# Performance work log

Hardware: AMD Instinct MI355X
Metric: run time of the kernel (lower is better)

The kernel has to match this reference:

```python
import jax, jax.numpy as jnp
import numpy as np

D_MODEL = 1024
NUM_HEADS = 16
HEAD_DIM = D_MODEL // NUM_HEADS
THETA = 10000.0
B, S = 2, 2048


def _apply_rope(t, cos, sin):
    # t: [B, H, S, hd]; cos/sin: [S, hd//2]
    te = t[..., 0::2]
    to = t[..., 1::2]
    re = te * cos - to * sin
    ro = te * sin + to * cos
    out = jnp.stack([re, ro], axis=-1)  # [B,H,S,hd//2,2]
    return out.reshape(t.shape)


def setup_inputs() -> dict:
    key = jax.random.key(0)
    kx, kq, kk, kv, ko = jax.random.split(key, 5)
    std = 2.0 / (2 * D_MODEL) ** 0.5
    def w(k):
        return jnp.clip(std * jax.random.normal(k, (D_MODEL, D_MODEL), jnp.float32), -3.0 * std, 3.0 * std)
    return {
        "x": jax.random.normal(kx, (B, S, D_MODEL), jnp.float32),
        "Wq": w(kq),
        "Wk": w(kk),
        "Wv": w(kv),
        "Wo": w(ko),
    }


def reference(x, Wq, Wk, Wv, Wo):
    Bv, Sv, _ = x.shape
    def proj(W):
        return jnp.einsum('bsd,ed->bse', x, W).reshape(Bv, Sv, NUM_HEADS, HEAD_DIM).transpose(0, 2, 1, 3)
    q, k, v = proj(Wq), proj(Wk), proj(Wv)

    pos = jnp.arange(Sv, dtype=jnp.float32)
    inv_freq = THETA ** (-jnp.arange(0, HEAD_DIM, 2, dtype=jnp.float32) / HEAD_DIM)
    ang = pos[:, None] * inv_freq[None, :]  # [S, hd//2]
    cos, sin = jnp.cos(ang), jnp.sin(ang)
    q = _apply_rope(q, cos, sin)
    k = _apply_rope(k, cos, sin)

    scale = 1.0 / jnp.sqrt(jnp.float32(HEAD_DIM))
    scores = jnp.einsum('bhqd,bhkd->bhqk', q.astype(jnp.float32), k.astype(jnp.float32)) * scale
    causal = jnp.tril(jnp.ones((Sv, Sv), dtype=bool))
    scores = jnp.where(causal[None, None], scores, -jnp.inf)
    attn = jax.nn.softmax(scores, axis=-1)
    out = jnp.einsum('bhqk,bhkd->bhqd', attn, v.astype(jnp.float32))
    out = out.transpose(0, 2, 1, 3).reshape(Bv, Sv, D_MODEL)
    return jnp.einsum('bsd,ed->bse', out, Wo)
```

## Files before the change

### kernel.cpp

```cpp
#include <hip/hip_runtime.h>
#include <hip/hip_bf16.h>
#include <stdint.h>

typedef __bf16 bf16x8 __attribute__((ext_vector_type(8)));
typedef float  f32x4  __attribute__((ext_vector_type(4)));

__device__ __forceinline__ float bf2f(unsigned short u) {
    union { float f; uint32_t i; } v; v.i = ((uint32_t)u) << 16; return v.f;
}
__device__ __forceinline__ unsigned short f2bf(float f) {
    union { float f; uint32_t i; } v; v.f = f;
    uint32_t r = v.i + 0x7FFF + ((v.i >> 16) & 1);
    return (unsigned short)(r >> 16);
}
__device__ __forceinline__ unsigned short f2bf_rz(float f) {
    union { float f; uint32_t i; } v; v.f = f;
    return (unsigned short)(v.i >> 16);
}
__device__ __forceinline__ float exp2_raw(float x) {
    float r;
    asm("v_exp_f32 %0, %1" : "=v"(r) : "v"(x));
    return r;
}

#define GLD_LDS(gptr, lptr) \
    __builtin_amdgcn_global_load_lds( \
        (const __attribute__((address_space(1))) void*)(gptr), \
        (__attribute__((address_space(3))) void*)(lptr), 16, 0, 0)

__global__ __launch_bounds__(256) void convert_inputs(
    const void* __restrict__ x,  const void* __restrict__ wq,
    const void* __restrict__ wk, const void* __restrict__ wv,
    const void* __restrict__ wo, unsigned short* __restrict__ dst,
    unsigned short* __restrict__ wob_dst, int* __restrict__ flag)
{
    __shared__ int cnt[256];
    const int tid = threadIdx.x;
    uint32_t u = ((const uint32_t*)x)[tid];
    int e = (u >> 7) & 0xFF;
    cnt[tid] = (e >= 100 && e <= 140) ? 1 : 0;
    __syncthreads();
    for (int s = 128; s > 0; s >>= 1) {
        if (tid < s) cnt[tid] += cnt[tid + s];
        __syncthreads();
    }
    const int isf32 = (cnt[0] >= 128) ? 0 : 1;
    if (blockIdx.x == 0 && tid == 0) flag[0] = isf32 ? 0 : 1;

    int c = blockIdx.x * 256 + tid;
    const void* src; size_t off; unsigned short* out;
    if (c < 524288)      { src = x;  off = (size_t)c * 8;            out = dst + (size_t)c * 8; }
    else if (c < 655360) { src = wq; off = (size_t)(c - 524288) * 8; out = dst + (size_t)c * 8; }
    else if (c < 786432) { src = wk; off = (size_t)(c - 655360) * 8; out = dst + (size_t)c * 8; }
    else if (c < 917504) { src = wv; off = (size_t)(c - 786432) * 8; out = dst + (size_t)c * 8; }
    else                 { src = wo; off = (size_t)(c - 917504) * 8; out = wob_dst + off; }
    unsigned short t[8];
    if (isf32) {
        const float* s = (const float*)src + off;
        float4 f0 = *(const float4*)s;
        float4 f1 = *(const float4*)(s + 4);
        t[0] = f2bf(f0.x); t[1] = f2bf(f0.y); t[2] = f2bf(f0.z); t[3] = f2bf(f0.w);
        t[4] = f2bf(f1.x); t[5] = f2bf(f1.y); t[6] = f2bf(f1.z); t[7] = f2bf(f1.w);
    } else {
        *(uint4*)t = *(const uint4*)((const unsigned short*)src + off);
    }
    *(uint4*)out = *(const uint4*)t;
}

__global__ __launch_bounds__(512, 2) void gemm_qkv_8ph(
    const unsigned short* __restrict__ A,
    const unsigned short* __restrict__ B0,
    const unsigned short* __restrict__ B1,
    const unsigned short* __restrict__ B2,
    unsigned short* __restrict__ O0,
    unsigned short* __restrict__ O1,
    unsigned short* __restrict__ O2)
{
    __shared__ __align__(16) unsigned short Asl[2][16384];
    __shared__ __align__(16) unsigned short Bsl[2][16384];

    const int tid  = threadIdx.x;
    const int lane = tid & 63;
    const int wid  = tid >> 6;
    const int wm   = wid >> 2;
    const int wn   = wid & 3;
    const int lr   = lane & 15;
    const int quad = lane >> 4;

    const int bid   = blockIdx.x;
    const int xcd   = bid & 7;
    const int s_    = bid >> 3;
    const int m_idx = xcd + 8 * (s_ / 12);
    const int n_idx = s_ % 12;

    const int m0  = m_idx * 256;
    const int n0g = n_idx * 256;
    const int sel = n0g >> 10;
    const unsigned short* Bp = (sel == 0) ? B0 : ((sel == 1) ? B1 : B2);
    unsigned short* Optr     = (sel == 0) ? O0 : ((sel == 1) ? O1 : O2);
    const int n0  = n0g & 1023;

    const int sw0 = ((0 + quad) ^ (lr & 7)) * 8;
    const int sw1 = ((4 + quad) ^ (lr & 7)) * 8;

    f32x4 acc[2][4][2][2] = {};
    bf16x8 aF[4][2];
    bf16x8 bF[2][2];

#define STAGEA(T, H) do { \
    const int tA_ = (T); \
    _Pragma("unroll") \
    for (int p_ = 0; p_ < 2; ++p_) { \
        int c_   = p_ * 512 + tid; \
        int row_ = c_ >> 3; \
        int sc_  = ((c_ & 7) ^ (row_ & 7)) * 8; \
        GLD_LDS(&A[(size_t)(m0 + (H) * 128 + row_) * 1024 + tA_ * 64 + sc_], \
                &Asl[tA_ & 1][(H) * 8192 + c_ * 8]); \
    } } while (0)

#define STAGEB(T, H) do { \
    const int tB_ = (T); \
    _Pragma("unroll") \
    for (int p_ = 0; p_ < 2; ++p_) { \
        int c_   = p_ * 512 + tid; \
        int row_ = c_ >> 3; \
        int sc_  = ((c_ & 7) ^ (row_ & 7)) * 8; \
        GLD_LDS(&Bp[(size_t)(n0 + (H) * 128 + row_) * 1024 + tB_ * 64 + sc_], \
                &Bsl[tB_ & 1][(H) * 8192 + c_ * 8]); \
    } } while (0)

#define LOADA(BUF, QM) do { \
    _Pragma("unroll") \
    for (int fm_ = 0; fm_ < 4; ++fm_) { \
        const int row_ = (QM) * 128 + wm * 64 + fm_ * 16 + lr; \
        aF[fm_][0] = *(const bf16x8*)&Asl[BUF][row_ * 64 + sw0]; \
        aF[fm_][1] = *(const bf16x8*)&Asl[BUF][row_ * 64 + sw1]; \
    } } while (0)

#define LOADB(BUF, QN) do { \
    _Pragma("unroll") \
    for (int fn_ = 0; fn_ < 2; ++fn_) { \
        const int row_ = (QN) * 128 + wn * 32 + fn_ * 16 + lr; \
        bF[fn_][0] = *(const bf16x8*)&Bsl[BUF][row_ * 64 + sw0]; \
        bF[fn_][1] = *(const bf16x8*)&Bsl[BUF][row_ * 64 + sw1]; \
    } } while (0)

#define MFMA16(QM, QN) do { \
    __builtin_amdgcn_s_setprio(1); \
    _Pragma("unroll") \
    for (int fm_ = 0; fm_ < 4; ++fm_) { \
        _Pragma("unroll") \
        for (int fn_ = 0; fn_ < 2; ++fn_) { \
            acc[QM][fm_][QN][fn_] = __builtin_amdgcn_mfma_f32_16x16x32_bf16( \
                aF[fm_][0], bF[fn_][0], acc[QM][fm_][QN][fn_], 0, 0, 0); \
            acc[QM][fm_][QN][fn_] = __builtin_amdgcn_mfma_f32_16x16x32_bf16( \
                aF[fm_][1], bF[fn_][1], acc[QM][fm_][QN][fn_], 0, 0, 0); \
        } \
    } \
    __builtin_amdgcn_s_setprio(0); \
    } while (0)

#define BARRIER() __builtin_amdgcn_s_barrier()
#define LGKM0()   asm volatile("s_waitcnt lgkmcnt(0)" ::: "memory")

    STAGEB(0, 0);
    STAGEA(0, 1);
    STAGEA(0, 0);
    STAGEB(0, 1);
    STAGEB(1, 0);
    STAGEA(1, 1);
    asm volatile("s_waitcnt vmcnt(4)" ::: "memory");
    BARRIER();

    const int NT = 16;
#pragma unroll 2
    for (int t = 0; t < NT; ++t) {
        const int buf = t & 1;

        LOADA(buf, 0);
        LOADB(buf, 0);
        if (t + 1 < NT) STAGEA(t + 1, 0);
        BARRIER();
        LGKM0();
        MFMA16(0, 0);
        BARRIER();

        LOADA(buf, 1);
        if (t + 1 < NT) STAGEB(t + 1, 1);
        BARRIER();
        LGKM0();
        MFMA16(1, 0);
        BARRIER();

        LOADB(buf, 1);
        if (t + 2 < NT) STAGEB(t + 2, 0);
        BARRIER();
        LGKM0();
        MFMA16(1, 1);
        BARRIER();

        LOADA(buf, 0);
        if (t + 2 < NT) STAGEA(t + 2, 1);
        BARRIER();
        LGKM0();
        MFMA16(0, 1);
        if (t + 2 < NT) asm volatile("s_waitcnt vmcnt(4)" ::: "memory");
        else            asm volatile("s_waitcnt vmcnt(0)" ::: "memory");
        BARRIER();
    }

#pragma unroll
    for (int qm = 0; qm < 2; ++qm) {
#pragma unroll
        for (int fm = 0; fm < 4; ++fm) {
            const int mb = m0 + qm * 128 + wm * 64 + fm * 16 + quad * 4;
#pragma unroll
            for (int qn = 0; qn < 2; ++qn) {
#pragma unroll
                for (int fn = 0; fn < 2; ++fn) {
                    const int nl = n0 + qn * 128 + wn * 32 + fn * 16 + lr;
                    const int h = nl >> 6, d = nl & 63;
#pragma unroll
                    for (int r = 0; r < 4; ++r) {
                        const int m = mb + r;
                        const int b = m >> 11, s = m & 2047;
                        Optr[((size_t)(b * 16 + h) * 2048 + s) * 64 + d] =
                            f2bf(acc[qm][fm][qn][fn][r]);
                    }
                }
            }
        }
    }
#undef STAGEA
#undef STAGEB
#undef LOADA
#undef LOADB
#undef MFMA16
#undef BARRIER
#undef LGKM0
}

template<int NS>
__global__ __launch_bounds__(256) void combine_kernel(
    const unsigned short* __restrict__ P0,
    const unsigned short* __restrict__ P1,
    const unsigned short* __restrict__ P2,
    const unsigned short* __restrict__ P3,
    const float* __restrict__ Lsum,
    unsigned short* __restrict__ C)
{
    const int tid = threadIdx.x;
    const int m   = blockIdx.x * 2 + (tid >> 7);
    const int c8  = (tid & 127) * 8;
    const int b = m >> 11, s = m & 2047;
    const int h = c8 >> 6, d0 = c8 & 63;
    const int li = (b * 16 + h) * 2048 + s;

    float lsum = Lsum[li] + Lsum[65536 + li];
    if (NS == 4) lsum += Lsum[131072 + li] + Lsum[196608 + li];
    const float inv = 1.0f / lsum;

    const size_t addr = (size_t)li * 64 + d0;
    unsigned short a[8], bb[8], o[8];
    *(uint4*)a  = *(const uint4*)&P0[addr];
    *(uint4*)bb = *(const uint4*)&P1[addr];
    if (NS == 4) {
        unsigned short c2[8], d2[8];
        *(uint4*)c2 = *(const uint4*)&P2[addr];
        *(uint4*)d2 = *(const uint4*)&P3[addr];
        for (int j = 0; j < 8; ++j)
            o[j] = f2bf((bf2f(a[j]) + bf2f(bb[j]) + bf2f(c2[j]) + bf2f(d2[j])) * inv);
    } else {
        for (int j = 0; j < 8; ++j)
            o[j] = f2bf((bf2f(a[j]) + bf2f(bb[j])) * inv);
    }
    *(uint4*)&C[(size_t)m * 1024 + c8] = *(const uint4*)o;
}

__global__ __launch_bounds__(256) void gemm_out(
    const unsigned short* __restrict__ A,
    const unsigned short* __restrict__ B0,
    void* __restrict__ O,
    const int* __restrict__ flag)
{
    const int K = 1024;
    __shared__ __align__(16) unsigned short As[64 * 64];
    __shared__ __align__(16) unsigned short Bs[128 * 64];

    const int isf32 = (flag[0] == 0) ? 1 : 0;

    const int tid  = threadIdx.x;
    const int lane = tid & 63;
    const int wid  = tid >> 6;
    const int wm   = wid >> 1;
    const int wn   = wid & 1;
    const int lr   = lane & 15;
    const int quad = lane >> 4;
    const int q8   = quad * 8;

    const int bid   = blockIdx.x;
    const int xcd   = bid & 7;
    const int s_    = bid >> 3;
    const int m_idx = xcd + 8 * (s_ >> 3);
    const int n_idx = s_ & 7;

    const int m0 = m_idx * 64;
    const int n0 = n_idx * 128;

    f32x4 acc[2][4] = {};

    for (int kk = 0; kk < K; kk += 64) {
        __syncthreads();
        for (int p = 0; p < 2; ++p) {
            int c   = p * 256 + tid;
            int row = c >> 3;
            int c8  = (c & 7) * 8;
            GLD_LDS(&A[(size_t)(m0 + row) * K + kk + c8], &As[c * 8]);
        }
        for (int p = 0; p < 4; ++p) {
            int c   = p * 256 + tid;
            int row = c >> 3;
            int c8  = (c & 7) * 8;
            GLD_LDS(&B0[(size_t)(n0 + row) * K + kk + c8], &Bs[c * 8]);
        }
        __syncthreads();

        for (int ks = 0; ks < 64; ks += 32) {
            bf16x8 af[2], bf[4];
            for (int t = 0; t < 2; ++t)
                af[t] = *(const bf16x8*)&As[(wm * 32 + t * 16 + lr) * 64 + ks + q8];
            for (int t = 0; t < 4; ++t)
                bf[t] = *(const bf16x8*)&Bs[(wn * 64 + t * 16 + lr) * 64 + ks + q8];
            for (int mt = 0; mt < 2; ++mt)
                for (int nt = 0; nt < 4; ++nt)
                    acc[mt][nt] = __builtin_amdgcn_mfma_f32_16x16x32_bf16(
                        af[mt], bf[nt], acc[mt][nt], 0, 0, 0);
        }
    }

    for (int mt = 0; mt < 2; ++mt) {
        for (int nt = 0; nt < 4; ++nt) {
            for (int r = 0; r < 4; ++r) {
                int m  = m0 + wm * 32 + mt * 16 + quad * 4 + r;
                int nl = n0 + wn * 64 + nt * 16 + lr;
                float val = acc[mt][nt][r];
                if (isf32) ((float*)O)[(size_t)m * 1024 + nl] = val;
                else ((unsigned short*)O)[(size_t)m * 1024 + nl] = f2bf(val);
            }
        }
    }
}

__global__ __launch_bounds__(256) void rope_transpose(
    unsigned short* __restrict__ Q, unsigned short* __restrict__ Kp,
    const unsigned short* __restrict__ V, unsigned short* __restrict__ Vt)
{
    __shared__ unsigned short T[64 * 65];
    const int tid = threadIdx.x;

    if (blockIdx.x < 4096) {
        const int CH = 32 * 2048 * 8;
        int idx = blockIdx.x * 256 + tid;
        bool isK = idx >= CH;
        int j = isK ? (idx - CH) : idx;
        unsigned short* p = isK ? Kp : Q;

        int c8   = j & 7;
        int srow = j >> 3;
        int s    = srow & 2047;
        int off  = srow * 64 + c8 * 8;

        uint4 raw = *(const uint4*)&p[off];
        unsigned short t[8];
        *(uint4*)t = raw;
        float sf = (float)s;
        float qs = isK ? 1.0f : 0.18033688011112043f;
        for (int jj = 0; jj < 4; ++jj) {
            int i = c8 * 4 + jj;
            float inv = __expf(-0.2878231366f * (float)i);
            float ang = sf * inv;
            float sn = __sinf(ang);
            float cs = __cosf(ang);
            float e = bf2f(t[2 * jj]);
            float o = bf2f(t[2 * jj + 1]);
            t[2 * jj]     = f2bf((e * cs - o * sn) * qs);
            t[2 * jj + 1] = f2bf((e * sn + o * cs) * qs);
        }
        *(uint4*)&p[off] = *(const uint4*)t;
    } else {
        int bidx = blockIdx.x - 4096;
        const int s0 = (bidx & 31) * 64;
        const int bh = bidx >> 5;

        const unsigned short* src = V + ((size_t)bh * 2048 + s0) * 64;
        for (int p = 0; p < 2; ++p) {
            int c = p * 256 + tid;
            int s  = c >> 3;
            int d8 = (c & 7) * 8;
            uint4 raw = *(const uint4*)&src[s * 64 + d8];
            unsigned short t[8];
            *(uint4*)t = raw;
            for (int j = 0; j < 8; ++j) T[s * 65 + d8 + j] = t[j];
        }
        __syncthreads();
        unsigned short* dst = Vt + (size_t)bh * 64 * 2048 + s0;
        for (int p = 0; p < 2; ++p) {
            int c = p * 256 + tid;
            int d  = c >> 3;
            int s8 = (c & 7) * 8;
            unsigned short t[8];
            for (int j = 0; j < 8; ++j) t[j] = T[(s8 + j) * 65 + d];
            *(uint4*)&dst[(size_t)d * 2048 + s8] = *(const uint4*)t;
        }
    }
}

__global__ __launch_bounds__(512) void attn_kernel512(
    const unsigned short* __restrict__ Q,
    const unsigned short* __restrict__ Kp,
    const unsigned short* __restrict__ Vt,
    unsigned short* __restrict__ P0,
    unsigned short* __restrict__ P1,
    unsigned short* __restrict__ P2,
    unsigned short* __restrict__ P3,
    float* __restrict__ Lsum)
{
    __shared__ __align__(16) unsigned short Ks[2][4096];
    __shared__ __align__(16) unsigned short Vs[2][4096];
    __shared__ __align__(16) unsigned short Ps[8192];

    const int tid  = threadIdx.x;
    const int lane = tid & 63;
    const int w    = tid >> 6;
    const int lr   = lane & 15;
    const int quad = lane >> 4;
    const int q8   = quad * 8;
    const int wps  = w * 1024;

    const int idx   = blockIdx.x;
    const int qb    = 7 - (idx >> 7);
    const int r_    = idx & 127;
    const int split = r_ >> 5;
    const int bh    = r_ & 31;
    const int kb0   = (qb + 1) * split;
    const int kb1   = (qb + 1) * (split + 1) - 1;

    unsigned short* Pout = (split == 0) ? P0 : (split == 1) ? P1
                         : (split == 2) ? P2 : P3;

    const unsigned short* KbBase = Kp + (size_t)bh * 2048 * 64;
    const unsigned short* VbBase = Vt + (size_t)bh * 131072;

    auto stage = [&](int kb, int buf) {
        const unsigned short* Kb = KbBase + kb * 64 * 64;
        const unsigned short* Vb = VbBase + kb * 64;
        int c    = tid;
        int f    = c >> 6, l = c & 63;
        int nt   = f >> 1, ks = f & 1;
        int lr_s = l & 15, qd = l >> 4;
        GLD_LDS(&Kb[(nt * 16 + lr_s) * 64 + ks * 32 + qd * 8], &Ks[buf][c * 8]);
        GLD_LDS(&Vb[(size_t)(nt * 16 + lr_s) * 2048 + ks * 32 + qd * 8], &Vs[buf][c * 8]);
    };

    const int q0 = qb * 256;
    bf16x8 qa[2][2];
    for (int mt = 0; mt < 2; ++mt) {
        const unsigned short* Qw = Q + ((size_t)bh * 2048 + q0 + w * 32 + mt * 16 + lr) * 64;
        qa[mt][0] = *(const bf16x8*)&Qw[q8];
        qa[mt][1] = *(const bf16x8*)&Qw[32 + q8];
    }

    stage(kb0, 0);

    f32x4 oacc[2][4] = {};
    float lpart[2][4] = {};
    const int l8 = lane * 8;
    const int lr7 = lr & 7;
    const int lrh = lr >> 3;

    for (int kb = kb0; kb <= kb1; ++kb) {
        const int cur = (kb - kb0) & 1;
        __syncthreads();
        if (kb < kb1) stage(kb + 1, cur ^ 1);

        f32x4 sacc[2][4] = {};
        for (int nt = 0; nt < 4; ++nt) {
            bf16x8 kf0 = *(const bf16x8*)&Ks[cur][(nt * 2 + 0) * 512 + l8];
            bf16x8 kf1 = *(const bf16x8*)&Ks[cur][(nt * 2 + 1) * 512 + l8];
            for (int mt = 0; mt < 2; ++mt) {
                sacc[mt][nt] = __builtin_amdgcn_mfma_f32_16x16x32_bf16(qa[mt][0], kf0, sacc[mt][nt], 0, 0, 0);
                sacc[mt][nt] = __builtin_amdgcn_mfma_f32_16x16x32_bf16(qa[mt][1], kf1, sacc[mt][nt], 0, 0, 0);
            }
        }

        if (kb >= 4 * qb) {
            for (int mt = 0; mt < 2; ++mt) {
                int rowb = q0 + w * 32 + mt * 16 + quad * 4;
                for (int nt = 0; nt < 4; ++nt) {
                    int col = kb * 64 + nt * 16 + lr;
                    for (int r = 0; r < 4; ++r)
                        if (col > rowb + r) sacc[mt][nt][r] = -3.0e38f;
                }
            }
        }

        for (int mt = 0; mt < 2; ++mt) {
            for (int r = 0; r < 4; ++r) {
                for (int nt = 0; nt < 4; ++nt) {
                    float pv = exp2_raw(sacc[mt][nt][r] - 23.083120654223414f);
                    lpart[mt][r] += pv;
                    int ks = nt >> 1;
                    int qr = (nt * 2 + lrh) & 3;
                    Ps[wps + ks * 512 + (qr * 16 + quad * 4 + r) * 8 + lr7] = f2bf_rz(pv);
                }
            }
            for (int ks = 0; ks < 2; ++ks) {
                bf16x8 pa = *(const bf16x8*)&Ps[wps + ks * 512 + l8];
                for (int nt = 0; nt < 4; ++nt) {
                    bf16x8 vf = *(const bf16x8*)&Vs[cur][(nt * 2 + ks) * 512 + l8];
                    oacc[mt][nt] = __builtin_amdgcn_mfma_f32_16x16x32_bf16(pa, vf, oacc[mt][nt], 0, 0, 0);
                }
            }
        }
    }

    for (int mt = 0; mt < 2; ++mt) {
        for (int r = 0; r < 4; ++r) {
            float l = lpart[mt][r];
            for (int off = 1; off < 16; off <<= 1)
                l += __shfl_xor(l, off, 64);
            int s = q0 + w * 32 + mt * 16 + quad * 4 + r;
            for (int nt = 0; nt < 4; ++nt)
                Pout[((size_t)bh * 2048 + s) * 64 + nt * 16 + lr] = f2bf_rz(oacc[mt][nt][r]);
            if (lr == 0) Lsum[split * 65536 + bh * 2048 + s] = l;
        }
    }
}

__global__ __launch_bounds__(256) void attn_kernel2(
    const unsigned short* __restrict__ Q,
    const unsigned short* __restrict__ Kp,
    const unsigned short* __restrict__ Vt,
    unsigned short* __restrict__ P0,
    unsigned short* __restrict__ P1,
    float* __restrict__ Lsum)
{
    __shared__ __align__(16) unsigned short Ks[2][4096];
    __shared__ __align__(16) unsigned short Vs[2][4096];
    __shared__ __align__(16) unsigned short Ps[4096];

    const int tid  = threadIdx.x;
    const int lane = tid & 63;
    const int w    = tid >> 6;
    const int lr   = lane & 15;
    const int quad = lane >> 4;
    const int q8   = quad * 8;
    const int wps  = w * 1024;

    const int bh    = blockIdx.x;
    const int y     = blockIdx.y;
    const int split = y >> 4;
    const int yq    = y & 15;
    const int qb    = (yq < 8) ? yq : (23 - yq);
    const int q0    = qb * 128;
    const int kb0   = split ? (qb + 1) : 0;
    const int kb1   = split ? (2 * qb + 1) : qb;

    unsigned short* Pout = split ? P1 : P0;

    const unsigned short* KbBase = Kp + (size_t)bh * 2048 * 64;
    const unsigned short* VbBase = Vt + (size_t)bh * 131072;

    auto stage = [&](int kb, int buf) {
        const unsigned short* Kb = KbBase + kb * 64 * 64;
        const unsigned short* Vb = VbBase + kb * 64;
        for (int p = 0; p < 2; ++p) {
            int c    = p * 256 + tid;
            int f    = c >> 6, l = c & 63;
            int nt   = f >> 1, ks = f & 1;
            int lr_s = l & 15, qd = l >> 4;
            GLD_LDS(&Kb[(nt * 16 + lr_s) * 64 + ks * 32 + qd * 8], &Ks[buf][c * 8]);
            GLD_LDS(&Vb[(size_t)(nt * 16 + lr_s) * 2048 + ks * 32 + qd * 8], &Vs[buf][c * 8]);
        }
    };

    bf16x8 qa[2][2];
    for (int mt = 0; mt < 2; ++mt) {
        const unsigned short* Qw = Q + ((size_t)bh * 2048 + q0 + mt * 64 + w * 16 + lr) * 64;
        qa[mt][0] = *(const bf16x8*)&Qw[q8];
        qa[mt][1] = *(const bf16x8*)&Qw[32 + q8];
    }

    stage(kb0, 0);

    f32x4 oacc[2][4] = {};
    float lpart[2][4] = {};
    const int l8 = lane * 8;
    const int lr7 = lr & 7;
    const int lrh = lr >> 3;

    for (int kb = kb0; kb <= kb1; ++kb) {
        const int cur = (kb - kb0) & 1;
        __syncthreads();
        if (kb < kb1) stage(kb + 1, cur ^ 1);

        f32x4 sacc[2][4] = {};
        for (int nt = 0; nt < 4; ++nt) {
            bf16x8 kf0 = *(const bf16x8*)&Ks[cur][(nt * 2 + 0) * 512 + l8];
            bf16x8 kf1 = *(const bf16x8*)&Ks[cur][(nt * 2 + 1) * 512 + l8];
            for (int mt = 0; mt < 2; ++mt) {
                sacc[mt][nt] = __builtin_amdgcn_mfma_f32_16x16x32_bf16(qa[mt][0], kf0, sacc[mt][nt], 0, 0, 0);
                sacc[mt][nt] = __builtin_amdgcn_mfma_f32_16x16x32_bf16(qa[mt][1], kf1, sacc[mt][nt], 0, 0, 0);
            }
        }

        if (kb >= 2 * qb) {
            for (int mt = 0; mt < 2; ++mt) {
                int rowb = q0 + mt * 64 + w * 16 + quad * 4;
                for (int nt = 0; nt < 4; ++nt) {
                    int col = kb * 64 + nt * 16 + lr;
                    for (int r = 0; r < 4; ++r)
                        if (col > rowb + r) sacc[mt][nt][r] = -3.0e38f;
                }
            }
        }

        for (int mt = 0; mt < 2; ++mt) {
            for (int r = 0; r < 4; ++r) {
                for (int nt = 0; nt < 4; ++nt) {
                    float pv = exp2_raw(sacc[mt][nt][r] - 23.083120654223414f);
                    lpart[mt][r] += pv;
                    int ks = nt >> 1;
                    int qr = (nt * 2 + lrh) & 3;
                    Ps[wps + ks * 512 + (qr * 16 + quad * 4 + r) * 8 + lr7] = f2bf_rz(pv);
                }
            }
            for (int ks = 0; ks < 2; ++ks) {
                bf16x8 pa = *(const bf16x8*)&Ps[wps + ks * 512 + l8];
                for (int nt = 0; nt < 4; ++nt) {
                    bf16x8 vf = *(const bf16x8*)&Vs[cur][(nt * 2 + ks) * 512 + l8];
                    oacc[mt][nt] = __builtin_amdgcn_mfma_f32_16x16x32_bf16(pa, vf, oacc[mt][nt], 0, 0, 0);
                }
            }
        }
    }

    for (int mt = 0; mt < 2; ++mt) {
        for (int r = 0; r < 4; ++r) {
            float l = lpart[mt][r];
            for (int off = 1; off < 16; off <<= 1)
                l += __shfl_xor(l, off, 64);
            int s = q0 + mt * 64 + w * 16 + quad * 4 + r;
            for (int nt = 0; nt < 4; ++nt)
                Pout[((size_t)bh * 2048 + s) * 64 + nt * 16 + lr] = f2bf_rz(oacc[mt][nt][r]);
            if (lr == 0) Lsum[split * 65536 + bh * 2048 + s] = l;
        }
    }
}

extern "C" void kernel_launch(void* const* d_in, const int* in_sizes, int n_in,
                              void* d_out, int out_size, void* d_ws, size_t ws_size,
                              hipStream_t stream)
{
    const void* x  = d_in[0];
    const void* Wq = d_in[1];
    const void* Wk = d_in[2];
    const void* Wv = d_in[3];
    const void* Wo = d_in[4];

    int* flag = (int*)d_ws;
    unsigned short* base = (unsigned short*)d_ws + 8;
    const size_t M1 = 1048576;
    unsigned short* xb  = base;
    unsigned short* wqb = base + 4 * M1;
    unsigned short* wkb = base + 5 * M1;
    unsigned short* wvb = base + 6 * M1;
    unsigned short* q   = base + 8 * M1;
    unsigned short* k   = base + 12 * M1;
    unsigned short* v   = base + 16 * M1;
    unsigned short* wob = base + 20 * M1;
    float*          Ls  = (float*)(base + 21 * M1);
    unsigned short* vt  = xb;
    unsigned short* P0  = v;
    unsigned short* P1  = wqb;
    unsigned short* P2  = base + 22 * M1;
    unsigned short* P3  = base + 26 * M1;
    unsigned short* Cb  = q;

    const bool big = ws_size >= (size_t)30 * M1 * 2 + 16;

    convert_inputs<<<dim3(4096), 256, 0, stream>>>(x, Wq, Wk, Wv, Wo, base, wob, flag);
    gemm_qkv_8ph<<<dim3(192), 512, 0, stream>>>(xb, wqb, wkb, wvb, q, k, v);
    rope_transpose<<<dim3(5120), 256, 0, stream>>>(q, k, v, vt);
    if (big) {
        attn_kernel512<<<dim3(1024), 512, 0, stream>>>(q, k, vt, P0, P1, P2, P3, Ls);
        combine_kernel<4><<<dim3(2048), 256, 0, stream>>>(P0, P1, P2, P3, Ls, Cb);
    } else {
        attn_kernel2<<<dim3(32, 32), 256, 0, stream>>>(q, k, vt, P0, P1, Ls);
        combine_kernel<2><<<dim3(2048), 256, 0, stream>>>(P0, P1, P0, P0, Ls, Cb);
    }
    gemm_out<<<dim3(512), 256, 0, stream>>>(Cb, wob, d_out, flag);
}
```

Measured before the change: 204.0 us.

## Split causal attention into fixed four-block KV chunks with eight partial buffers

Adds a new attention work decomposition in which each block handles a fixed chunk of four KV tiles, so row block qb gets qb+1 chunks (36 chunks per head, 1152 blocks). Before, each query block was split into four equal parts whose size grew with qb. The combine kernel gains an eight-way path that sums only the partials valid for each query row block. The goal is uniform per-block work and better load balance across CUs. The cost is more partial output traffic and a workspace requirement of about 46M elements; if the workspace is smaller, the code falls back to the previous paths.

Result: no change. 206.0 us (+0.9%).

```diff
diff --git a/kernel.cpp b/kernel.cpp
--- a/kernel.cpp
+++ b/kernel.cpp
@@ -246,6 +246,10 @@
     const unsigned short* __restrict__ P1,
     const unsigned short* __restrict__ P2,
     const unsigned short* __restrict__ P3,
+    const unsigned short* __restrict__ P4,
+    const unsigned short* __restrict__ P5,
+    const unsigned short* __restrict__ P6,
+    const unsigned short* __restrict__ P7,
     const float* __restrict__ Lsum,
     unsigned short* __restrict__ C)
 {
@@ -255,24 +259,42 @@
     const int b = m >> 11, s = m & 2047;
     const int h = c8 >> 6, d0 = c8 & 63;
     const int li = (b * 16 + h) * 2048 + s;
-
-    float lsum = Lsum[li] + Lsum[65536 + li];
-    if (NS == 4) lsum += Lsum[131072 + li] + Lsum[196608 + li];
-    const float inv = 1.0f / lsum;
-
     const size_t addr = (size_t)li * 64 + d0;
-    unsigned short a[8], bb[8], o[8];
-    *(uint4*)a  = *(const uint4*)&P0[addr];
-    *(uint4*)bb = *(const uint4*)&P1[addr];
-    if (NS == 4) {
-        unsigned short c2[8], d2[8];
-        *(uint4*)c2 = *(const uint4*)&P2[addr];
-        *(uint4*)d2 = *(const uint4*)&P3[addr];
-        for (int j = 0; j < 8; ++j)
-            o[j] = f2bf((bf2f(a[j]) + bf2f(bb[j]) + bf2f(c2[j]) + bf2f(d2[j])) * inv);
+
+    unsigned short o[8];
+    if (NS == 8) {
+        const int qbrow = s >> 8;
+        const unsigned short* Ptab[8] = {P0, P1, P2, P3, P4, P5, P6, P7};
+        float lsum = 0.0f;
+        float of[8] = {};
+#pragma unroll
+        for (int c = 0; c < 8; ++c) {
+            if (c <= qbrow) {
+                lsum += Lsum[c * 65536 + li];
+                unsigned short a[8];
+                *(uint4*)a = *(const uint4*)&Ptab[c][addr];
+                for (int j = 0; j < 8; ++j) of[j] += bf2f(a[j]);
+            }
+        }
+        const float inv = 1.0f / lsum;
+        for (int j = 0; j < 8; ++j) o[j] = f2bf(of[j] * inv);
     } else {
-        for (int j = 0; j < 8; ++j)
-            o[j] = f2bf((bf2f(a[j]) + bf2f(bb[j])) * inv);
+        float lsum = Lsum[li] + Lsum[65536 + li];
+        if (NS == 4) lsum += Lsum[131072 + li] + Lsum[196608 + li];
+        const float inv = 1.0f / lsum;
+        unsigned short a[8], bb[8];
+        *(uint4*)a  = *(const uint4*)&P0[addr];
+        *(uint4*)bb = *(const uint4*)&P1[addr];
+        if (NS == 4) {
+            unsigned short c2[8], d2[8];
+            *(uint4*)c2 = *(const uint4*)&P2[addr];
+            *(uint4*)d2 = *(const uint4*)&P3[addr];
+            for (int j = 0; j < 8; ++j)
+                o[j] = f2bf((bf2f(a[j]) + bf2f(bb[j]) + bf2f(c2[j]) + bf2f(d2[j])) * inv);
+        } else {
+            for (int j = 0; j < 8; ++j)
+                o[j] = f2bf((bf2f(a[j]) + bf2f(bb[j])) * inv);
+        }
     }
     *(uint4*)&C[(size_t)m * 1024 + c8] = *(const uint4*)o;
 }
@@ -415,6 +437,7 @@
     }
 }
 
+template<int MODE>
 __global__ __launch_bounds__(512) void attn_kernel512(
     const unsigned short* __restrict__ Q,
     const unsigned short* __restrict__ Kp,
@@ -423,6 +446,10 @@
     unsigned short* __restrict__ P1,
     unsigned short* __restrict__ P2,
     unsigned short* __restrict__ P3,
+    unsigned short* __restrict__ P4,
+    unsigned short* __restrict__ P5,
+    unsigned short* __restrict__ P6,
+    unsigned short* __restrict__ P7,
     float* __restrict__ Lsum)
 {
     __shared__ __align__(16) unsigned short Ks[2][4096];
@@ -437,16 +464,34 @@
     const int q8   = quad * 8;
     const int wps  = w * 1024;
 
-    const int idx   = blockIdx.x;
-    const int qb    = 7 - (idx >> 7);
-    const int r_    = idx & 127;
-    const int split = r_ >> 5;
-    const int bh    = r_ & 31;
-    const int kb0   = (qb + 1) * split;
-    const int kb1   = (qb + 1) * (split + 1) - 1;
-
-    unsigned short* Pout = (split == 0) ? P0 : (split == 1) ? P1
-                         : (split == 2) ? P2 : P3;
+    const int idx = blockIdx.x;
+    int qb, sel, bh, kb0, kb1;
+    if (MODE == 0) {
+        qb  = 7 - (idx >> 7);
+        const int r_ = idx & 127;
+        sel = r_ >> 5;
+        bh  = r_ & 31;
+        kb0 = (qb + 1) * sel;
+        kb1 = (qb + 1) * (sel + 1) - 1;
+    } else {
+        bh = idx & 31;
+        const int cid = idx >> 5;
+        if      (cid < 8)  { qb = 7; sel = cid; }
+        else if (cid < 15) { qb = 6; sel = cid - 8; }
+        else if (cid < 21) { qb = 5; sel = cid - 15; }
+        else if (cid < 26) { qb = 4; sel = cid - 21; }
+        else if (cid < 30) { qb = 3; sel = cid - 26; }
+        else if (cid < 33) { qb = 2; sel = cid - 30; }
+        else if (cid < 35) { qb = 1; sel = cid - 33; }
+        else               { qb = 0; sel = 0; }
+        kb0 = sel * 4;
+        kb1 = kb0 + 3;
+    }
+
+    unsigned short* Pout = (sel == 0) ? P0 : (sel == 1) ? P1
+                         : (sel == 2) ? P2 : (sel == 3) ? P3
+                         : (sel == 4) ? P4 : (sel == 5) ? P5
+                         : (sel == 6) ? P6 : P7;
 
     const unsigned short* KbBase = Kp + (size_t)bh * 2048 * 64;
     const unsigned short* VbBase = Vt + (size_t)bh * 131072;
@@ -532,7 +577,7 @@
             int s = q0 + w * 32 + mt * 16 + quad * 4 + r;
             for (int nt = 0; nt < 4; ++nt)
                 Pout[((size_t)bh * 2048 + s) * 64 + nt * 16 + lr] = f2bf_rz(oacc[mt][nt][r]);
-            if (lr == 0) Lsum[split * 65536 + bh * 2048 + s] = l;
+            if (lr == 0) Lsum[sel * 65536 + bh * 2048 + s] = l;
         }
     }
 }
@@ -685,19 +730,32 @@
     unsigned short* P1  = wqb;
     unsigned short* P2  = base + 22 * M1;
     unsigned short* P3  = base + 26 * M1;
+    unsigned short* P4  = base + 30 * M1;
+    unsigned short* P5  = base + 34 * M1;
+    unsigned short* P6  = base + 38 * M1;
+    unsigned short* P7  = base + 42 * M1;
     unsigned short* Cb  = q;
 
-    const bool big = ws_size >= (size_t)30 * M1 * 2 + 16;
+    const bool big8 = ws_size >= (size_t)46 * M1 * 2 + 16;
+    const bool big4 = ws_size >= (size_t)30 * M1 * 2 + 16;
 
     convert_inputs<<<dim3(4096), 256, 0, stream>>>(x, Wq, Wk, Wv, Wo, base, wob, flag);
     gemm_qkv_8ph<<<dim3(192), 512, 0, stream>>>(xb, wqb, wkb, wvb, q, k, v);
     rope_transpose<<<dim3(5120), 256, 0, stream>>>(q, k, v, vt);
-    if (big) {
-        attn_kernel512<<<dim3(1024), 512, 0, stream>>>(q, k, vt, P0, P1, P2, P3, Ls);
-        combine_kernel<4><<<dim3(2048), 256, 0, stream>>>(P0, P1, P2, P3, Ls, Cb);
+    if (big8) {
+        attn_kernel512<1><<<dim3(1152), 512, 0, stream>>>(
+            q, k, vt, P0, P1, P2, P3, P4, P5, P6, P7, Ls);
+        combine_kernel<8><<<dim3(2048), 256, 0, stream>>>(
+            P0, P1, P2, P3, P4, P5, P6, P7, Ls, Cb);
+    } else if (big4) {
+        attn_kernel512<0><<<dim3(1024), 512, 0, stream>>>(
+            q, k, vt, P0, P1, P2, P3, P0, P0, P0, P0, Ls);
+        combine_kernel<4><<<dim3(2048), 256, 0, stream>>>(
+            P0, P1, P2, P3, P0, P0, P0, P0, Ls, Cb);
     } else {
         attn_kernel2<<<dim3(32, 32), 256, 0, stream>>>(q, k, vt, P0, P1, Ls);
-        combine_kernel<2><<<dim3(2048), 256, 0, stream>>>(P0, P1, P0, P0, Ls, Cb);
+        combine_kernel<2><<<dim3(2048), 256, 0, stream>>>(
+            P0, P1, P0, P0, P0, P0, P0, P0, Ls, Cb);
     }
     gemm_out<<<dim3(512), 256, 0, stream>>>(Cb, wob, d_out, flag);
 }
```
